# Optimization experiments

Measured on AMD Instinct MI355X. Metric: run time of the kernel, lower is better.

The kernel has to match this reference:

```python
import jax, jax.numpy as jnp
import numpy as np

N_NODES = 100000
N_EDGES = 1280000
IN_DIM = 256
OUT_DIM = 64


def setup_inputs() -> dict:
    key = jax.random.key(0)
    k1, k2, k3, k4, k5, k6 = jax.random.split(key, 6)
    x = jax.random.normal(k1, (N_NODES, IN_DIM), dtype=jnp.float32)
    support_rows = jax.random.randint(k2, (N_EDGES,), 0, N_NODES, dtype=jnp.int64)
    support_cols = jax.random.randint(k3, (N_EDGES,), 0, N_NODES, dtype=jnp.int64)
    support_vals = jax.random.uniform(k4, (N_EDGES,), dtype=jnp.float32)
    weight = jax.random.normal(k5, (IN_DIM, OUT_DIM), dtype=jnp.float32) * 0.05
    bias = jax.random.normal(k6, (OUT_DIM,), dtype=jnp.float32) * 0.05
    return {
        "x": x,
        "support_rows": support_rows,
        "support_cols": support_cols,
        "support_vals": support_vals,
        "weight": weight,
        "bias": bias,
    }


def reference(x, support_rows, support_cols, support_vals, weight, bias):
    # dropout=0, training=False -> dropout is identity
    # pre_sup = X @ W : [N, out_dim]
    pre_sup = jnp.matmul(x, weight)
    # sparse support (COO) @ pre_sup : gather source rows, scale, scatter-add to dest rows
    gathered = pre_sup[support_cols] * support_vals[:, None]  # [E, out_dim]
    out = jax.ops.segment_sum(gathered, support_rows, num_segments=N_NODES)
    out = out + bias
    return jax.nn.relu(out)
```

## Files before the change

kernel.cpp:

```cpp
#include <hip/hip_runtime.h>
#include <hip/hip_bf16.h>
#include <stdint.h>

#define N_NODES 100000
#define N_EDGES 1280000
#define IN_DIM  256
#define OUT_DIM 64
#define NB1     98
#define GEMM_BLOCKS ((N_NODES + 63) / 64)

#define HSL   4
#define HSB   25000
#define HCH   50
#define HEPC  (N_EDGES / HCH)

#define RSL   8
#define RSN   (N_NODES / RSL)

typedef __attribute__((ext_vector_type(8))) short bf16x8;
typedef __attribute__((ext_vector_type(4))) float f32x4;
typedef __attribute__((ext_vector_type(4))) unsigned short u16x4;
typedef __attribute__((ext_vector_type(4))) int i32x4;

__device__ __forceinline__ unsigned short f32_to_bf16(float f) {
    union { float f; unsigned int u; } c; c.f = f;
    unsigned int u = c.u;
    u += 0x7fffu + ((u >> 16) & 1u);
    return (unsigned short)(u >> 16);
}
__device__ __forceinline__ float bf16_to_f32(unsigned short h) {
    union { unsigned int u; float f; } c; c.u = ((unsigned int)h) << 16; return c.f;
}

__global__ __launch_bounds__(256) void wpack_kernel(const float* __restrict__ w,
                                                    unsigned short* __restrict__ wbf) {
    const int i0 = blockIdx.x * 1024;
    for (int i = i0 + threadIdx.x; i < i0 + 1024; i += 256) {
        const int k = i >> 6, n = i & 63;
        const int kt = k >> 5, q = (k >> 3) & 3, j = k & 7;
        const int t = n >> 4, l = n & 15;
        wbf[((kt * 4 + t) * 64 + q * 16 + l) * 8 + j] = f32_to_bf16(w[i]);
    }
}

__global__ __launch_bounds__(256) void hist_kernel(const int* __restrict__ rows,
                                                   unsigned short* __restrict__ partial) {
    __shared__ unsigned int lh[HSB / 2];
    const int s = blockIdx.x & 3;
    const int c = blockIdx.x >> 2;
    const int lo = s * HSB;
    for (int i = threadIdx.x; i < HSB / 2; i += 256) lh[i] = 0u;
    __syncthreads();
    const i32x4* rp = (const i32x4*)(rows + c * HEPC);
    for (int i = threadIdx.x; i < HEPC / 4; i += 256) {
        const i32x4 r4 = rp[i];
        const unsigned d0 = (unsigned)(r4.x - lo);
        const unsigned d1 = (unsigned)(r4.y - lo);
        const unsigned d2 = (unsigned)(r4.z - lo);
        const unsigned d3 = (unsigned)(r4.w - lo);
        if (d0 < HSB) atomicAdd(&lh[d0 >> 1], 1u << ((d0 & 1) * 16));
        if (d1 < HSB) atomicAdd(&lh[d1 >> 1], 1u << ((d1 & 1) * 16));
        if (d2 < HSB) atomicAdd(&lh[d2 >> 1], 1u << ((d2 & 1) * 16));
        if (d3 < HSB) atomicAdd(&lh[d3 >> 1], 1u << ((d3 & 1) * 16));
    }
    __syncthreads();
    unsigned int* dst = (unsigned int*)(partial + (size_t)c * N_NODES + lo);
    for (int i = threadIdx.x; i < HSB / 2; i += 256) dst[i] = lh[i];
}

__global__ __launch_bounds__(256, 4) void gemm_kernel(const float* __restrict__ x,
                                                      const unsigned short* __restrict__ wbf,
                                                      unsigned short* __restrict__ pre) {
    __shared__ __align__(16) unsigned short wt[IN_DIM * OUT_DIM];

    const int tid = threadIdx.x;
    const int wave = tid >> 6;
    const int lane = tid & 63;
    const int ln16 = lane & 15;
    const int quad = lane >> 4;

    const int R0 = blockIdx.x * 64;
    const int arow = R0 + wave * 16 + ln16;
    const float* xrow = x + (size_t)(arow < N_NODES ? arow : N_NODES - 1) * IN_DIM + quad * 8;

    f32x4 xa[8], xb[8];
    #pragma unroll
    for (int kt = 0; kt < 8; ++kt) {
        xa[kt] = *(const f32x4*)(xrow + kt * 32);
        xb[kt] = *(const f32x4*)(xrow + kt * 32 + 4);
    }

    #pragma unroll
    for (int i = 0; i < 8; ++i)
        *(bf16x8*)&wt[i * 2048 + tid * 8] = *(const bf16x8*)(wbf + i * 2048 + tid * 8);

    __syncthreads();

    f32x4 acc[4] = {};

    #pragma unroll
    for (int kt = 0; kt < 8; ++kt) {
        bf16x8 a;
        a[0] = (short)f32_to_bf16(xa[kt].x); a[1] = (short)f32_to_bf16(xa[kt].y);
        a[2] = (short)f32_to_bf16(xa[kt].z); a[3] = (short)f32_to_bf16(xa[kt].w);
        a[4] = (short)f32_to_bf16(xb[kt].x); a[5] = (short)f32_to_bf16(xb[kt].y);
        a[6] = (short)f32_to_bf16(xb[kt].z); a[7] = (short)f32_to_bf16(xb[kt].w);
        #pragma unroll
        for (int t = 0; t < 4; ++t) {
            bf16x8 b = *(const bf16x8*)&wt[((kt * 4 + t) * 64 + lane) * 8];
            acc[t] = __builtin_amdgcn_mfma_f32_16x16x32_bf16(a, b, acc[t], 0, 0, 0);
        }
    }

    const int rbase = R0 + wave * 16 + quad * 4;
    #pragma unroll
    for (int t = 0; t < 4; ++t) {
        #pragma unroll
        for (int r = 0; r < 4; ++r) {
            const int rr = rbase + r;
            if (rr < N_NODES)
                pre[(size_t)rr * OUT_DIM + t * 16 + ln16] = f32_to_bf16(acc[t][r]);
        }
    }
}

__global__ __launch_bounds__(256) void scan1_kernel(const unsigned short* __restrict__ partial,
                                                    int* __restrict__ off,
                                                    int* __restrict__ bsum) {
    __shared__ int s[256];
    const int t = threadIdx.x;
    const int base = blockIdx.x * 1024 + t * 4;
    int d[4] = {0, 0, 0, 0};
    for (int c = 0; c < HCH; ++c) {
        const u16x4 v = *(const u16x4*)(partial + (size_t)c * N_NODES + base);
        d[0] += v[0]; d[1] += v[1]; d[2] += v[2]; d[3] += v[3];
    }
    #pragma unroll
    for (int q = 0; q < 4; ++q)
        if (base + q >= N_NODES) d[q] = 0;
    const int tsum = d[0] + d[1] + d[2] + d[3];
    s[t] = tsum;
    __syncthreads();
    #pragma unroll
    for (int o = 1; o < 256; o <<= 1) {
        const int add = t >= o ? s[t - o] : 0;
        __syncthreads();
        s[t] += add;
        __syncthreads();
    }
    int run = t > 0 ? s[t - 1] : 0;
    #pragma unroll
    for (int q = 0; q < 4; ++q) {
        const int i = base + q;
        if (i < N_NODES) off[i] = run;
        run += d[q];
    }
    if (t == 255) bsum[blockIdx.x] = run;
}

__global__ __launch_bounds__(128) void scan2_kernel(const int* __restrict__ bsum,
                                                    int* __restrict__ boff,
                                                    int* __restrict__ off) {
    __shared__ int s[128];
    const int t = threadIdx.x;
    const int v = t < NB1 ? bsum[t] : 0;
    s[t] = v;
    __syncthreads();
    #pragma unroll
    for (int o = 1; o < 128; o <<= 1) {
        const int add = t >= o ? s[t - o] : 0;
        __syncthreads();
        s[t] += add;
        __syncthreads();
    }
    if (t < NB1) boff[t] = t > 0 ? s[t - 1] : 0;
    if (t == 127) off[N_NODES] = s[127];
}

__global__ __launch_bounds__(256) void scan3_kernel(int* __restrict__ off,
                                                    const int* __restrict__ boff,
                                                    int* __restrict__ cursor) {
    const int i = blockIdx.x * 256 + threadIdx.x;
    if (i < N_NODES) {
        const int v = off[i] + boff[i >> 10];
        off[i] = v;
        cursor[i] = v;
    }
}

__global__ __launch_bounds__(512) void reorder_kernel(const int* __restrict__ rows,
                                                      const int* __restrict__ cols,
                                                      const float* __restrict__ vals,
                                                      int* __restrict__ cursor,
                                                      unsigned long long* __restrict__ epack) {
    const int s = blockIdx.x & 7;
    const int c = blockIdx.x >> 3;
    const int lo = s * RSN;
    const i32x4* rp = (const i32x4*)(rows + c * HEPC);
    const int nq = HEPC / 4;
    for (int i = threadIdx.x; i < nq; i += 512) {
        const i32x4 r4 = __builtin_nontemporal_load(rp + i);
        const int e0 = c * HEPC + i * 4;
        #pragma unroll
        for (int k = 0; k < 4; ++k) {
            const int r = r4[k];
            const unsigned d = (unsigned)(r - lo);
            if (d < RSN) {
                const int cc = __builtin_nontemporal_load(cols + e0 + k);
                const float vv = __builtin_nontemporal_load(vals + e0 + k);
                const int slot = atomicAdd(&cursor[r], 1);
                epack[slot] = ((unsigned long long)__float_as_uint(vv) << 32) | (unsigned int)cc;
            }
        }
    }
}

__global__ __launch_bounds__(256) void gather_kernel(const int* __restrict__ off,
                                                     const unsigned long long* __restrict__ epack,
                                                     const unsigned short* __restrict__ pre,
                                                     const float* __restrict__ bias,
                                                     float* __restrict__ out) {
    const int v = blockIdx.x * 4 + (threadIdx.x >> 6);
    const int j = threadIdx.x & 63;
    if (v >= N_NODES) return;
    const int s = off[v];
    const int e = off[v + 1];
    float acc = 0.0f;
    int i = s;
    for (; i + 4 <= e; i += 4) {
        unsigned long long ee[4];
        float p[4];
        #pragma unroll
        for (int q = 0; q < 4; ++q) ee[q] = epack[i + q];
        #pragma unroll
        for (int q = 0; q < 4; ++q)
            p[q] = bf16_to_f32(pre[(size_t)(unsigned int)(ee[q] & 0xffffffffu) * OUT_DIM + j]);
        #pragma unroll
        for (int q = 0; q < 4; ++q)
            acc = fmaf(p[q], __uint_as_float((unsigned int)(ee[q] >> 32)), acc);
    }
    for (; i < e; ++i) {
        const unsigned long long e0 = epack[i];
        acc = fmaf(bf16_to_f32(pre[(size_t)(unsigned int)(e0 & 0xffffffffu) * OUT_DIM + j]),
                   __uint_as_float((unsigned int)(e0 >> 32)), acc);
    }
    const float r = acc + bias[j];
    out[(size_t)v * OUT_DIM + j] = r > 0.0f ? r : 0.0f;
}

extern "C" void kernel_launch(void* const* d_in, const int* in_sizes, int n_in,
                              void* d_out, int out_size, void* d_ws, size_t ws_size,
                              hipStream_t stream) {
    const float* x    = (const float*)d_in[0];
    const int* rows   = (const int*)d_in[1];
    const int* cols   = (const int*)d_in[2];
    const float* vals = (const float*)d_in[3];
    const float* w    = (const float*)d_in[4];
    const float* bias = (const float*)d_in[5];
    float* out        = (float*)d_out;

    unsigned short* pre = (unsigned short*)d_ws;
    int* off    = (int*)(pre + (size_t)N_NODES * OUT_DIM);
    int* cursor = off + N_NODES + 4;
    int* bsum   = cursor + N_NODES;
    int* boff   = bsum + 128;
    unsigned long long* epack = (unsigned long long*)(boff + 128);

    unsigned short* partial = (unsigned short*)epack;
    unsigned short* wbf = (unsigned short*)cursor;

    wpack_kernel<<<16, 256, 0, stream>>>(w, wbf);

    hist_kernel<<<HSL * HCH, 256, 0, stream>>>(rows, partial);

    gemm_kernel<<<GEMM_BLOCKS, 256, 0, stream>>>(x, wbf, pre);

    scan1_kernel<<<NB1, 256, 0, stream>>>(partial, off, bsum);
    scan2_kernel<<<1, 128, 0, stream>>>(bsum, boff, off);
    scan3_kernel<<<(N_NODES + 255) / 256, 256, 0, stream>>>(off, boff, cursor);

    reorder_kernel<<<RSL * HCH, 512, 0, stream>>>(rows, cols, vals, cursor, epack);

    gather_kernel<<<(N_NODES + 3) / 4, 256, 0, stream>>>(off, epack, pre, bias, out);
}
```

Before: 341.5 us.

## Replace global atomic cursors with per-chunk prefix offsets and LDS-local rank atomics

scan1 now writes, for each edge chunk, the exclusive running count per node into a u16 array kept in the output buffer. The reorder kernel computes each edge's slot as the node offset plus that chunk's prefix plus a rank from an LDS atomic over its node slice. This replaces contended global atomics on a cursor array, and nontemporal loads become plain loads. The cost is a 10 MB extra write in scan1, extra reads of off and cumt in reorder, and a 50 KB LDS array that limits occupancy. The LDS rank also makes the order within a chunk nondeterministic.

```diff
diff --git a/kernel.cpp b/kernel.cpp
--- a/kernel.cpp
+++ b/kernel.cpp
@@ -125,14 +125,27 @@
 }
 
 __global__ __launch_bounds__(256) void scan1_kernel(const unsigned short* __restrict__ partial,
+                                                    unsigned short* __restrict__ cumt,
                                                     int* __restrict__ off,
                                                     int* __restrict__ bsum) {
     __shared__ int s[256];
     const int t = threadIdx.x;
     const int base = blockIdx.x * 1024 + t * 4;
+    const bool full = (base + 4 <= N_NODES);
     int d[4] = {0, 0, 0, 0};
     for (int c = 0; c < HCH; ++c) {
         const u16x4 v = *(const u16x4*)(partial + (size_t)c * N_NODES + base);
+        if (full) {
+            u16x4 pk;
+            pk[0] = (unsigned short)d[0]; pk[1] = (unsigned short)d[1];
+            pk[2] = (unsigned short)d[2]; pk[3] = (unsigned short)d[3];
+            *(u16x4*)(cumt + (size_t)c * N_NODES + base) = pk;
+        } else {
+            #pragma unroll
+            for (int q = 0; q < 4; ++q)
+                if (base + q < N_NODES)
+                    cumt[(size_t)c * N_NODES + base + q] = (unsigned short)d[q];
+        }
         d[0] += v[0]; d[1] += v[1]; d[2] += v[2]; d[3] += v[3];
     }
     #pragma unroll
@@ -178,37 +191,38 @@
 }
 
 __global__ __launch_bounds__(256) void scan3_kernel(int* __restrict__ off,
-                                                    const int* __restrict__ boff,
-                                                    int* __restrict__ cursor) {
+                                                    const int* __restrict__ boff) {
     const int i = blockIdx.x * 256 + threadIdx.x;
-    if (i < N_NODES) {
-        const int v = off[i] + boff[i >> 10];
-        off[i] = v;
-        cursor[i] = v;
-    }
+    if (i < N_NODES) off[i] += boff[i >> 10];
 }
 
 __global__ __launch_bounds__(512) void reorder_kernel(const int* __restrict__ rows,
                                                       const int* __restrict__ cols,
                                                       const float* __restrict__ vals,
-                                                      int* __restrict__ cursor,
+                                                      const int* __restrict__ off,
+                                                      const unsigned short* __restrict__ cumt,
                                                       unsigned long long* __restrict__ epack) {
+    __shared__ unsigned int lcur[RSN];
     const int s = blockIdx.x & 7;
     const int c = blockIdx.x >> 3;
     const int lo = s * RSN;
+    for (int i = threadIdx.x; i < RSN; i += 512) lcur[i] = 0u;
+    __syncthreads();
     const i32x4* rp = (const i32x4*)(rows + c * HEPC);
+    const unsigned short* cumc = cumt + (size_t)c * N_NODES;
     const int nq = HEPC / 4;
     for (int i = threadIdx.x; i < nq; i += 512) {
-        const i32x4 r4 = __builtin_nontemporal_load(rp + i);
+        const i32x4 r4 = rp[i];
         const int e0 = c * HEPC + i * 4;
         #pragma unroll
         for (int k = 0; k < 4; ++k) {
             const int r = r4[k];
             const unsigned d = (unsigned)(r - lo);
             if (d < RSN) {
-                const int cc = __builtin_nontemporal_load(cols + e0 + k);
-                const float vv = __builtin_nontemporal_load(vals + e0 + k);
-                const int slot = atomicAdd(&cursor[r], 1);
+                const int cc = cols[e0 + k];
+                const float vv = vals[e0 + k];
+                const unsigned rank = atomicAdd(&lcur[d], 1u);
+                const int slot = off[r] + (int)cumc[r] + (int)rank;
                 epack[slot] = ((unsigned long long)__float_as_uint(vv) << 32) | (unsigned int)cc;
             }
         }
@@ -268,6 +282,7 @@
 
     unsigned short* partial = (unsigned short*)epack;
     unsigned short* wbf = (unsigned short*)cursor;
+    unsigned short* cumt = (unsigned short*)out;
 
     wpack_kernel<<<16, 256, 0, stream>>>(w, wbf);
 
@@ -275,11 +290,11 @@
 
     gemm_kernel<<<GEMM_BLOCKS, 256, 0, stream>>>(x, wbf, pre);
 
-    scan1_kernel<<<NB1, 256, 0, stream>>>(partial, off, bsum);
+    scan1_kernel<<<NB1, 256, 0, stream>>>(partial, cumt, off, bsum);
     scan2_kernel<<<1, 128, 0, stream>>>(bsum, boff, off);
-    scan3_kernel<<<(N_NODES + 255) / 256, 256, 0, stream>>>(off, boff, cursor);
-
-    reorder_kernel<<<RSL * HCH, 512, 0, stream>>>(rows, cols, vals, cursor, epack);
+    scan3_kernel<<<(N_NODES + 255) / 256, 256, 0, stream>>>(off, boff);
+
+    reorder_kernel<<<RSL * HCH, 512, 0, stream>>>(rows, cols, vals, off, cumt, epack);
 
     gather_kernel<<<(N_NODES + 3) / 4, 256, 0, stream>>>(off, epack, pre, bias, out);
 }
```

Measured after the change: 328.7 us. 3.7% less time.
